# Performance work log

Measured on AMD Instinct MI355X. Metric: run time of the kernel, lower is better.

The kernel has to match this reference:

```python
import jax, jax.numpy as jnp
import numpy as np

B, N, K, E, H, V = 128, 256, 4, 300, 150, 32000  # batch, nodes/tree, max children, embed, hidden, vocab
DELTA = 1.0


def setup_inputs() -> dict:
    key = jax.random.key(0)
    ks = jax.random.split(key, 8)
    query = jax.random.randint(ks[0], (B, N), 0, V, dtype=jnp.int32)
    pos = jax.random.randint(ks[1], (B, N), 0, V, dtype=jnp.int32)
    neg = jax.random.randint(ks[2], (B, N), 0, V, dtype=jnp.int32)
    # Complete K-ary tree over N nodes: children of node t are {K*t+1, ..., K*t+K} < N; root = node 0.
    ch = np.full((N, K), -1, dtype=np.int32)
    for t in range(N):
        for j in range(K):
            c = K * t + 1 + j
            if c < N:
                ch[t, j] = c
    children = jnp.asarray(ch)
    emb = jax.random.normal(ks[3], (V, E), dtype=jnp.float32) * 0.02
    W_iou = jax.random.normal(ks[4], (E, 3 * H), dtype=jnp.float32) * 0.05
    U_iou = jax.random.normal(ks[5], (H, 3 * H), dtype=jnp.float32) * 0.05
    b_iou = jnp.zeros((3 * H,), jnp.float32)
    W_f = jax.random.normal(ks[6], (E, H), dtype=jnp.float32) * 0.05
    U_f = jax.random.normal(ks[7], (H, H), dtype=jnp.float32) * 0.05
    b_f = jnp.zeros((H,), jnp.float32)
    return {"query": query, "pos": pos, "neg": neg, "children": children,
            "emb": emb, "W_iou": W_iou, "U_iou": U_iou, "b_iou": b_iou,
            "W_f": W_f, "U_f": U_f, "b_f": b_f}


def _childsum_treelstm(x, children, W_iou, U_iou, b_iou, W_f, U_f, b_f):
    """x: [B, N, E] node embeddings. Returns root (c, h): each [B, H]."""
    Bn, Nn, _ = x.shape
    Hh = U_f.shape[0]
    h0 = jnp.zeros((Bn, Nn, Hh), x.dtype)
    c0 = jnp.zeros((Bn, Nn, Hh), x.dtype)

    def step(carry, t):
        h_all, c_all = carry
        ch = children[t]                        # [K] child indices, -1 = padding
        mask = (ch >= 0)
        idx = jnp.where(mask, ch, 0)
        m = mask.astype(x.dtype)[None, :, None]  # [1, K, 1]
        h_k = h_all[:, idx] * m                 # [B, K, H]
        c_k = c_all[:, idx] * m
        h_sum = h_k.sum(axis=1)                 # child-sum h_tilde [B, H]
        x_t = x[:, t]                           # [B, E]
        iou = x_t @ W_iou + h_sum @ U_iou + b_iou
        i, o, u = jnp.split(iou, 3, axis=-1)
        i = jax.nn.sigmoid(i)
        o = jax.nn.sigmoid(o)
        u = jnp.tanh(u)
        # per-child forget gates: f_jk = sigmoid(W_f x_j + U_f h_k + b_f)
        f = jax.nn.sigmoid((x_t @ W_f + b_f)[:, None, :] + h_k @ U_f)  # [B, K, H]
        c_t = i * u + (f * c_k).sum(axis=1)     # c_k already masked
        h_t = o * jnp.tanh(c_t)
        return (h_all.at[:, t].set(h_t), c_all.at[:, t].set(c_t)), None

    # children have larger indices than parents -> process N-1 .. 0 (root last)
    (h_all, c_all), _ = jax.lax.scan(step, (h0, c0), jnp.arange(Nn - 1, -1, -1))
    return c_all[:, 0], h_all[:, 0]


def _cosine(a, b):
    num = (a * b).sum(-1)
    den = jnp.sqrt((a * a).sum(-1) * (b * b).sum(-1)) + 1e-8
    return num / den


def reference(query, pos, neg, children, emb, W_iou, U_iou, b_iou, W_f, U_f, b_f):
    qc, _ = _childsum_treelstm(emb[query], children, W_iou, U_iou, b_iou, W_f, U_f, b_f)
    pc, _ = _childsum_treelstm(emb[pos], children, W_iou, U_iou, b_iou, W_f, U_f, b_f)
    nc, _ = _childsum_treelstm(emb[neg], children, W_iou, U_iou, b_iou, W_f, U_f, b_f)
    a = _cosine(qc, pc)  # [B]
    b = _cosine(qc, nc)  # [B]
    return jax.nn.relu(DELTA - a + b)
```

## Files before the change

kernel.cpp:

```cpp
#include <hip/hip_runtime.h>
#include <hip/hip_bf16.h>

typedef short short8 __attribute__((ext_vector_type(8)));
typedef float floatx4 __attribute__((ext_vector_type(4)));
typedef unsigned short ushort;

#define Bb 128
#define Nn 256
#define Hh 150
#define HK 160
#define Vv 32000
#define NROW 384
#define PROJC 600
#define NINT 64
#define ZROW (Vv + NROW * NINT)

#define WTN 640

__device__ __forceinline__ float sigf(float x) { return 1.0f / (1.0f + __expf(-x)); }
__device__ __forceinline__ float tanhf_(float x) { return 1.0f - 2.0f / (__expf(2.0f * x) + 1.0f); }
__device__ __forceinline__ float bf2f(ushort s) { union { float f; unsigned u; } v; v.u = ((unsigned)s) << 16; return v.f; }
__device__ __forceinline__ ushort f2bf(float f) { __hip_bfloat16 h = __float2bfloat16(f); return *(ushort*)&h; }

__global__ __launch_bounds__(256) void k_prep(
    const float* __restrict__ W_iou, const float* __restrict__ W_f,
    const float* __restrict__ U_iou, const float* __restrict__ U_f,
    const float* __restrict__ b_iou, const float* __restrict__ b_f,
    short* __restrict__ Wt, short* __restrict__ Uti, short* __restrict__ Utf,
    float* __restrict__ biasw, ushort* __restrict__ h_u, float* __restrict__ c_u)
{
    int idx = blockIdx.x * 256 + threadIdx.x;
    const int nWt = 320 * WTN, nUi = 160 * 464, nUf = 160 * 160;
    if (idx < nWt) {
        int k = idx / WTN, n = idx % WTN;
        float v = 0.f;
        if (k < 300) { if (n < 450) v = W_iou[k * 450 + n]; else if (n < 600) v = W_f[k * 150 + (n - 450)]; }
        Wt[n * 320 + k] = (short)f2bf(v);
    } else if (idx < nWt + nUi) {
        int i2 = idx - nWt; int k = i2 / 464, n = i2 % 464;
        float v = (k < 150 && n < 450) ? U_iou[k * 450 + n] : 0.f;
        Uti[n * 160 + k] = (short)f2bf(v);
    } else if (idx < nWt + nUi + nUf) {
        int i2 = idx - nWt - nUi; int k = i2 / 160, n = i2 % 160;
        float v = (k < 150 && n < 150) ? U_f[k * 150 + n] : 0.f;
        Utf[n * 160 + k] = (short)f2bf(v);
    } else if (idx < nWt + nUi + nUf + WTN) {
        int n = idx - nWt - nUi - nUf;
        biasw[n] = n < 450 ? b_iou[n] : (n < 600 ? b_f[n - 450] : 0.f);
    } else if (idx < nWt + nUi + nUf + WTN + HK) {
        int k = idx - (nWt + nUi + nUf + WTN);
        h_u[(long)ZROW * HK + k] = 0;
        c_u[(long)ZROW * HK + k] = 0.f;
    }
}

__global__ __launch_bounds__(256) void k_vproj(
    const float* __restrict__ emb, const short* __restrict__ Wt,
    const float* __restrict__ biasw, ushort* __restrict__ proj)
{
    __shared__ __align__(16) short As[2][32][328];
    const int tid = threadIdx.x;

    const int bid = blockIdx.x;
    const int xcd = bid & 7, li = bid >> 3;
    const int wgid = (xcd < 4 ? xcd * 63 : 252 + (xcd - 4) * 62) + li;

    const int cg = wgid % 5;
    const int rg = wgid / 5;
    const int rowbase = rg * 320;

    const int w = tid >> 6, lane = tid & 63;
    const int m = lane & 15, kq = (lane >> 4) * 8;
    const int t0 = cg * 8 + w * 2;
    const int col0 = t0 * 16 + m;
    const int col1 = col0 + 16;

    short8 bq0[10], bq1[10];
    #pragma unroll
    for (int ks = 0; ks < 10; ks++) {
        bq0[ks] = *(const short8*)(Wt + (long)col0 * 320 + kq + ks * 32);
        bq1[ks] = *(const short8*)(Wt + (long)col1 * 320 + kq + ks * 32);
    }
    const float bias0 = biasw[col0];
    const float bias1 = biasw[col1];

    for (int i = tid; i < 2 * 32 * 5; i += 256) {
        int bz = i / 160, r2 = (i % 160) / 5, kk = (i % 5) * 4;
        *(short4*)&As[bz][r2][300 + kk] = make_short4(0, 0, 0, 0);
    }

    {
        const float4* src = (const float4*)emb + (long)rowbase * 75;
        for (int i = tid; i < 2400; i += 256) {
            int r = i / 75, k0 = (i % 75) * 4;
            float4 x = src[i];
            short4 sv;
            sv.x = (short)f2bf(x.x); sv.y = (short)f2bf(x.y);
            sv.z = (short)f2bf(x.z); sv.w = (short)f2bf(x.w);
            *(short4*)&As[0][r][k0] = sv;
        }
    }
    __syncthreads();

    for (int c = 0; c < 10; c++) {
        const int buf = c & 1;

        float4 x[10];
        if (c < 9) {
            const float4* src = (const float4*)emb + (long)(rowbase + (c + 1) * 32) * 75;
            #pragma unroll
            for (int j = 0; j < 10; j++) {
                int i = tid + j * 256;
                if (i < 2400) x[j] = src[i];
            }
        }

        floatx4 a00 = {0.f,0.f,0.f,0.f}, a01 = a00, a10 = a00, a11 = a00;
        #pragma unroll
        for (int ks = 0; ks < 10; ks++) {
            short8 a0 = *(const short8*)&As[buf][m][kq + ks * 32];
            short8 a1 = *(const short8*)&As[buf][16 + m][kq + ks * 32];
            a00 = __builtin_amdgcn_mfma_f32_16x16x32_bf16(a0, bq0[ks], a00, 0, 0, 0);
            a01 = __builtin_amdgcn_mfma_f32_16x16x32_bf16(a0, bq1[ks], a01, 0, 0, 0);
            a10 = __builtin_amdgcn_mfma_f32_16x16x32_bf16(a1, bq0[ks], a10, 0, 0, 0);
            a11 = __builtin_amdgcn_mfma_f32_16x16x32_bf16(a1, bq1[ks], a11, 0, 0, 0);
        }

        {
            int v0 = rowbase + c * 32;
            int rb = (lane >> 4) * 4;
            if (col0 < PROJC) {
                #pragma unroll
                for (int reg = 0; reg < 4; reg++) {
                    proj[(long)(v0 + rb + reg) * PROJC + col0]      = f2bf(a00[reg] + bias0);
                    proj[(long)(v0 + 16 + rb + reg) * PROJC + col0] = f2bf(a10[reg] + bias0);
                }
            }
            if (col1 < PROJC) {
                #pragma unroll
                for (int reg = 0; reg < 4; reg++) {
                    proj[(long)(v0 + rb + reg) * PROJC + col1]      = f2bf(a01[reg] + bias1);
                    proj[(long)(v0 + 16 + rb + reg) * PROJC + col1] = f2bf(a11[reg] + bias1);
                }
            }
        }

        if (c < 9) {
            #pragma unroll
            for (int j = 0; j < 10; j++) {
                int i = tid + j * 256;
                if (i < 2400) {
                    int r = i / 75, k0 = (i % 75) * 4;
                    short4 sv;
                    sv.x = (short)f2bf(x[j].x); sv.y = (short)f2bf(x[j].y);
                    sv.z = (short)f2bf(x[j].z); sv.w = (short)f2bf(x[j].w);
                    *(short4*)&As[buf ^ 1][r][k0] = sv;
                }
            }
        }
        __syncthreads();
    }
}

__global__ __launch_bounds__(256) void k_vleaf(
    const ushort* __restrict__ proj, ushort* __restrict__ h_u, float* __restrict__ c_u)
{
    int idx = blockIdx.x * 256 + threadIdx.x;
    int v = idx / 20, k0 = (idx % 20) * 8;
    const ushort* pr = proj + (long)v * PROJC;
    ushort hv[8]; float cvv[8];
    #pragma unroll
    for (int e = 0; e < 8; e++) {
        int k = k0 + e;
        if (k < Hh) {
            float iv = sigf(bf2f(pr[k]));
            float ov = sigf(bf2f(pr[150 + k]));
            float uv = tanhf_(bf2f(pr[300 + k]));
            float cc = iv * uv;
            cvv[e] = cc;
            hv[e] = f2bf(ov * tanhf_(cc));
        } else { cvv[e] = 0.f; hv[e] = 0; }
    }
    *(int4*)(h_u + (long)v * HK + k0) = *(int4*)hv;
    *(float4*)(c_u + (long)v * HK + k0)     = make_float4(cvv[0], cvv[1], cvv[2], cvv[3]);
    *(float4*)(c_u + (long)v * HK + k0 + 4) = make_float4(cvv[4], cvv[5], cvv[6], cvv[7]);
}

template<int CB>
__device__ __forceinline__ void level_step(
    int tA, int nT, int r0, int cb,
    const int* __restrict__ tq, const int* __restrict__ tp, const int* __restrict__ tn,
    const int* __restrict__ children, const ushort* __restrict__ proj,
    const short* __restrict__ Uti, const short* __restrict__ Utf,
    ushort* __restrict__ h_u, float* __restrict__ c_u,
    short (*As)[16][168], ushort (*idx_s)[16][4], ushort (*tok_s)[16])
{
    const int tid = threadIdx.x;

    if (tid < 64 * nT) {
        int tt = tid >> 6, q = tid & 63;
        int r = q >> 2, j = q & 3;
        int t = tA + tt;
        int rg = r0 + r, g = rg >> 7, b = rg & 127;
        const int* tok = (g == 0) ? tq : (g == 1 ? tp : tn);
        int ch = children[t * 4 + j];
        int idx;
        if (ch < 0)        idx = ZROW;
        else if (ch >= 64) idx = tok[b * Nn + ch];
        else               idx = Vv + rg * NINT + ch;
        idx_s[tt][r][j] = (ushort)idx;
        if (j == 0) tok_s[tt][r] = (ushort)tok[b * Nn + t];
    }
    __syncthreads();

    for (int i = tid; i < 320 * nT; i += 256) {
        int tt = i / 320, i2 = i % 320;
        int r = i2 / 20, k0 = (i2 % 20) * 8;
        int4 v0 = *(const int4*)(h_u + (long)idx_s[tt][r][0] * HK + k0);
        int4 v1 = *(const int4*)(h_u + (long)idx_s[tt][r][1] * HK + k0);
        int4 v2 = *(const int4*)(h_u + (long)idx_s[tt][r][2] * HK + k0);
        int4 v3 = *(const int4*)(h_u + (long)idx_s[tt][r][3] * HK + k0);
        *(int4*)&As[tt * 5 + 1][r][k0] = v0;
        *(int4*)&As[tt * 5 + 2][r][k0] = v1;
        *(int4*)&As[tt * 5 + 3][r][k0] = v2;
        *(int4*)&As[tt * 5 + 4][r][k0] = v3;
        ushort s[8];
        const ushort* p0 = (const ushort*)&v0; const ushort* p1 = (const ushort*)&v1;
        const ushort* p2 = (const ushort*)&v2; const ushort* p3 = (const ushort*)&v3;
        #pragma unroll
        for (int e = 0; e < 8; e++)
            s[e] = f2bf(bf2f(p0[e]) + bf2f(p1[e]) + bf2f(p2[e]) + bf2f(p3[e]));
        *(int4*)&As[tt * 5 + 0][r][k0] = *(int4*)s;
    }
    __syncthreads();

    const int w = tid >> 6, lane = tid & 63;
    const int m = lane & 15, kq = (lane >> 4) * 8;
    const int rbase = (lane >> 4) * 4;

    for (int nt = w + 4 * cb; nt < 10; nt += 4 * CB) {
        int col = nt * 16 + m;

        short8 Bi[5], Bo[5], Bu[5], Bf[5];
        #pragma unroll
        for (int ks = 0; ks < 5; ks++) {
            Bi[ks] = *(const short8*)(Uti + (long)(col)       * HK + kq + ks * 32);
            Bo[ks] = *(const short8*)(Uti + (long)(150 + col) * HK + kq + ks * 32);
            Bu[ks] = *(const short8*)(Uti + (long)(300 + col) * HK + kq + ks * 32);
            Bf[ks] = *(const short8*)(Utf + (long)(col)       * HK + kq + ks * 32);
        }

        for (int tt = 0; tt < nT; ++tt) {
            int t = tA + tt;

            float pv0[4], pv1[4], pv2[4], pv3[4];
            float cu0[4], cu1[4], cu2[4], cu3[4];
            if (col < Hh) {
                #pragma unroll
                for (int reg = 0; reg < 4; reg++) {
                    const ushort* pr = proj + (long)tok_s[tt][rbase + reg] * PROJC;
                    pv0[reg] = bf2f(pr[col]);
                    pv1[reg] = bf2f(pr[150 + col]);
                    pv2[reg] = bf2f(pr[300 + col]);
                    pv3[reg] = bf2f(pr[450 + col]);
                    cu0[reg] = c_u[(long)idx_s[tt][rbase + reg][0] * HK + col];
                    cu1[reg] = c_u[(long)idx_s[tt][rbase + reg][1] * HK + col];
                    cu2[reg] = c_u[(long)idx_s[tt][rbase + reg][2] * HK + col];
                    cu3[reg] = c_u[(long)idx_s[tt][rbase + reg][3] * HK + col];
                }
            }

            floatx4 ai = {0.f,0.f,0.f,0.f}, ao = ai, au = ai;
            floatx4 af0 = ai, af1 = ai, af2 = ai, af3 = ai;
            #pragma unroll
            for (int ks = 0; ks < 5; ks++) {
                short8 asum = *(const short8*)&As[tt * 5 + 0][m][kq + ks * 32];
                short8 ac0  = *(const short8*)&As[tt * 5 + 1][m][kq + ks * 32];
                short8 ac1  = *(const short8*)&As[tt * 5 + 2][m][kq + ks * 32];
                short8 ac2  = *(const short8*)&As[tt * 5 + 3][m][kq + ks * 32];
                short8 ac3  = *(const short8*)&As[tt * 5 + 4][m][kq + ks * 32];
                ai  = __builtin_amdgcn_mfma_f32_16x16x32_bf16(asum, Bi[ks], ai, 0, 0, 0);
                ao  = __builtin_amdgcn_mfma_f32_16x16x32_bf16(asum, Bo[ks], ao, 0, 0, 0);
                au  = __builtin_amdgcn_mfma_f32_16x16x32_bf16(asum, Bu[ks], au, 0, 0, 0);
                af0 = __builtin_amdgcn_mfma_f32_16x16x32_bf16(ac0,  Bf[ks], af0, 0, 0, 0);
                af1 = __builtin_amdgcn_mfma_f32_16x16x32_bf16(ac1,  Bf[ks], af1, 0, 0, 0);
                af2 = __builtin_amdgcn_mfma_f32_16x16x32_bf16(ac2,  Bf[ks], af2, 0, 0, 0);
                af3 = __builtin_amdgcn_mfma_f32_16x16x32_bf16(ac3,  Bf[ks], af3, 0, 0, 0);
            }

            if (col < Hh) {
                #pragma unroll
                for (int reg = 0; reg < 4; reg++) {
                    int rg = r0 + rbase + reg;
                    float iv = sigf(pv0[reg] + ai[reg]);
                    float ov = sigf(pv1[reg] + ao[reg]);
                    float uv = tanhf_(pv2[reg] + au[reg]);
                    float fpre = pv3[reg];
                    float cv = iv * uv;
                    cv = fmaf(sigf(fpre + af0[reg]), cu0[reg], cv);
                    cv = fmaf(sigf(fpre + af1[reg]), cu1[reg], cv);
                    cv = fmaf(sigf(fpre + af2[reg]), cu2[reg], cv);
                    cv = fmaf(sigf(fpre + af3[reg]), cu3[reg], cv);
                    long o = (long)(Vv + rg * NINT + t) * HK + col;
                    c_u[o] = cv;
                    h_u[o] = f2bf(ov * tanhf_(cv));
                }
            } else {
                #pragma unroll
                for (int reg = 0; reg < 4; reg++) {
                    long o = (long)(Vv + (r0 + rbase + reg) * NINT + t) * HK + col;
                    c_u[o] = 0.f; h_u[o] = 0;
                }
            }
        }
    }
}

template<int CB>
__global__ __launch_bounds__(256) void k_level(
    int t_base, int t_cnt,
    const int* __restrict__ tq, const int* __restrict__ tp, const int* __restrict__ tn,
    const int* __restrict__ children, const ushort* __restrict__ proj,
    const short* __restrict__ Uti, const short* __restrict__ Utf,
    ushort* __restrict__ h_u, float* __restrict__ c_u)
{
    __shared__ __align__(16) short As[10][16][168];
    __shared__ ushort idx_s[2][16][4];
    __shared__ ushort tok_s[2][16];

    const int chunk = blockIdx.x / (24 * CB);
    const int rem   = blockIdx.x % (24 * CB);
    const int r0 = (rem / CB) * 16;
    const int cb = rem % CB;
    const int tA = t_base + chunk * 2;
    const int nT = min(2, t_base + t_cnt - tA);

    level_step<CB>(tA, nT, r0, cb, tq, tp, tn, children, proj, Uti, Utf,
                   h_u, c_u, As, idx_s, tok_s);
}

__global__ __launch_bounds__(64) void k_cos(const float* __restrict__ c_u, float* __restrict__ out)
{
    int b = blockIdx.x, tid = threadIdx.x;
    const float* qc = c_u + (long)(Vv + (0 * Bb + b) * NINT) * HK;
    const float* pc = c_u + (long)(Vv + (1 * Bb + b) * NINT) * HK;
    const float* nc = c_u + (long)(Vv + (2 * Bb + b) * NINT) * HK;
    float qp = 0, qn = 0, qq = 0, pp = 0, nn2 = 0;
    for (int k = tid; k < Hh; k += 64) {
        float qv = qc[k], pv = pc[k], nv = nc[k];
        qp += qv * pv; qn += qv * nv; qq += qv * qv; pp += pv * pv; nn2 += nv * nv;
    }
    #pragma unroll
    for (int off = 32; off > 0; off >>= 1) {
        qp += __shfl_down(qp, off, 64);
        qn += __shfl_down(qn, off, 64);
        qq += __shfl_down(qq, off, 64);
        pp += __shfl_down(pp, off, 64);
        nn2 += __shfl_down(nn2, off, 64);
    }
    if (tid == 0) {
        float a = qp / (sqrtf(qq * pp) + 1e-8f);
        float d = qn / (sqrtf(qq * nn2) + 1e-8f);
        out[b] = fmaxf(0.0f, 1.0f - a + d);
    }
}

extern "C" void kernel_launch(void* const* d_in, const int* in_sizes, int n_in,
                              void* d_out, int out_size, void* d_ws, size_t ws_size,
                              hipStream_t stream)
{
    const int*   tq       = (const int*)d_in[0];
    const int*   tp       = (const int*)d_in[1];
    const int*   tn       = (const int*)d_in[2];
    const int*   children = (const int*)d_in[3];
    const float* emb      = (const float*)d_in[4];
    const float* W_iou    = (const float*)d_in[5];
    const float* U_iou    = (const float*)d_in[6];
    const float* b_iou    = (const float*)d_in[7];
    const float* W_f      = (const float*)d_in[8];
    const float* U_f      = (const float*)d_in[9];
    const float* b_f      = (const float*)d_in[10];
    float* out = (float*)d_out;

    char* ws = (char*)d_ws;
    ushort* proj  = (ushort*)ws;
    ushort* h_u   = (ushort*)(ws + 38400000);
    float*  c_u   = (float*)(ws + 56504640);
    short*  Wt    = (short*)(ws + 92713920);
    short*  Uti   = (short*)(ws + 93123520);
    short*  Utf   = (short*)(ws + 93272000);
    float*  biasw = (float*)(ws + 93323200);

    k_prep<<<1194, 256, 0, stream>>>(W_iou, W_f, U_iou, U_f, b_iou, b_f,
                                     Wt, Uti, Utf, biasw, h_u, c_u);
    k_vproj<<<500, 256, 0, stream>>>(emb, Wt, biasw, proj);
    k_vleaf<<<2500, 256, 0, stream>>>(proj, h_u, c_u);
    k_level<1><<<22 * 24, 256, 0, stream>>>(21, 43, tq, tp, tn, children, proj, Uti, Utf, h_u, c_u);
    k_level<1><<<8 * 24, 256, 0, stream>>>(5, 16, tq, tp, tn, children, proj, Uti, Utf, h_u, c_u);
    k_level<2><<<2 * 24 * 2, 256, 0, stream>>>(1, 4, tq, tp, tn, children, proj, Uti, Utf, h_u, c_u);
    k_level<2><<<1 * 24 * 2, 256, 0, stream>>>(0, 1, tq, tp, tn, children, proj, Uti, Utf, h_u, c_u);
    k_cos<<<Bb, 64, 0, stream>>>(c_u, out);
}
```

Before: 240.8 us.

## Interleave projection gate columns and fuse leaf LSTM cell into vocab projection GEMM

Reorders the projected weight columns so the i/o/u/f gates of each hidden unit sit next to each other. The vocab-projection kernel can then compute leaf cell and hidden states in its epilogue using lane shuffles, and the separate leaf kernel and its re-read of the projection table are removed. The level kernel now reads all four gate values for a node with one short4 load instead of four scattered loads. The cost is extra transcendental work and scattered 4-byte stores in the GEMM epilogue, which could lengthen that kernel.

```diff
diff --git a/kernel.cpp b/kernel.cpp
--- a/kernel.cpp
+++ b/kernel.cpp
@@ -17,6 +17,7 @@
 
 #define WTN 640
 
+
 __device__ __forceinline__ float sigf(float x) { return 1.0f / (1.0f + __expf(-x)); }
 __device__ __forceinline__ float tanhf_(float x) { return 1.0f - 2.0f / (__expf(2.0f * x) + 1.0f); }
 __device__ __forceinline__ float bf2f(ushort s) { union { float f; unsigned u; } v; v.u = ((unsigned)s) << 16; return v.f; }
@@ -32,10 +33,12 @@
     int idx = blockIdx.x * 256 + threadIdx.x;
     const int nWt = 320 * WTN, nUi = 160 * 464, nUf = 160 * 160;
     if (idx < nWt) {
-        int k = idx / WTN, n = idx % WTN;
+        int kk = idx / WTN, c = idx % WTN;
+        int k = c >> 2, g = c & 3;
         float v = 0.f;
-        if (k < 300) { if (n < 450) v = W_iou[k * 450 + n]; else if (n < 600) v = W_f[k * 150 + (n - 450)]; }
-        Wt[n * 320 + k] = (short)f2bf(v);
+        if (kk < 300 && k < 150)
+            v = (g < 3) ? W_iou[kk * 450 + g * 150 + k] : W_f[kk * 150 + k];
+        Wt[c * 320 + kk] = (short)f2bf(v);
     } else if (idx < nWt + nUi) {
         int i2 = idx - nWt; int k = i2 / 464, n = i2 % 464;
         float v = (k < 150 && n < 450) ? U_iou[k * 450 + n] : 0.f;
@@ -45,8 +48,9 @@
         float v = (k < 150 && n < 150) ? U_f[k * 150 + n] : 0.f;
         Utf[n * 160 + k] = (short)f2bf(v);
     } else if (idx < nWt + nUi + nUf + WTN) {
-        int n = idx - nWt - nUi - nUf;
-        biasw[n] = n < 450 ? b_iou[n] : (n < 600 ? b_f[n - 450] : 0.f);
+        int c = idx - nWt - nUi - nUf;
+        int k = c >> 2, g = c & 3;
+        biasw[c] = (k < 150) ? (g < 3 ? b_iou[g * 150 + k] : b_f[k]) : 0.f;
     } else if (idx < nWt + nUi + nUf + WTN + HK) {
         int k = idx - (nWt + nUi + nUf + WTN);
         h_u[(long)ZROW * HK + k] = 0;
@@ -56,7 +60,8 @@
 
 __global__ __launch_bounds__(256) void k_vproj(
     const float* __restrict__ emb, const short* __restrict__ Wt,
-    const float* __restrict__ biasw, ushort* __restrict__ proj)
+    const float* __restrict__ biasw, ushort* __restrict__ proj,
+    ushort* __restrict__ h_u, float* __restrict__ c_u)
 {
     __shared__ __align__(16) short As[2][32][328];
     const int tid = threadIdx.x;
@@ -74,6 +79,9 @@
     const int t0 = cg * 8 + w * 2;
     const int col0 = t0 * 16 + m;
     const int col1 = col0 + 16;
+    const int g = m & 3;
+    const int k0 = t0 * 4 + (m >> 2);
+    const int rb = (lane >> 4) * 4;
 
     short8 bq0[10], bq1[10];
     #pragma unroll
@@ -92,12 +100,12 @@
     {
         const float4* src = (const float4*)emb + (long)rowbase * 75;
         for (int i = tid; i < 2400; i += 256) {
-            int r = i / 75, k0 = (i % 75) * 4;
+            int r = i / 75, kk0 = (i % 75) * 4;
             float4 x = src[i];
             short4 sv;
             sv.x = (short)f2bf(x.x); sv.y = (short)f2bf(x.y);
             sv.z = (short)f2bf(x.z); sv.w = (short)f2bf(x.w);
-            *(short4*)&As[0][r][k0] = sv;
+            *(short4*)&As[0][r][kk0] = sv;
         }
     }
     __syncthreads();
@@ -126,9 +134,9 @@
             a11 = __builtin_amdgcn_mfma_f32_16x16x32_bf16(a1, bq1[ks], a11, 0, 0, 0);
         }
 
+        const int v0 = rowbase + c * 32;
+
         {
-            int v0 = rowbase + c * 32;
-            int rb = (lane >> 4) * 4;
             if (col0 < PROJC) {
                 #pragma unroll
                 for (int reg = 0; reg < 4; reg++) {
@@ -145,45 +153,60 @@
             }
         }
 
+        #pragma unroll
+        for (int reg = 0; reg < 4; reg++) {
+            float vA = a00[reg] + bias0;
+            float vB = a10[reg] + bias0;
+            float vC = a01[reg] + bias1;
+            float vD = a11[reg] + bias1;
+            float A1 = __shfl_xor(vA, 1), A2 = __shfl_xor(vA, 2), A3 = __shfl_xor(vA, 3);
+            float B1 = __shfl_xor(vB, 1), B2 = __shfl_xor(vB, 2), B3 = __shfl_xor(vB, 3);
+            float C1 = __shfl_xor(vC, 1), C2 = __shfl_xor(vC, 2), C3 = __shfl_xor(vC, 3);
+            float D1 = __shfl_xor(vD, 1), D2 = __shfl_xor(vD, 2), D3 = __shfl_xor(vD, 3);
+            if (g < 2) {
+                int r0w = v0 + rb + reg, r1w = v0 + 16 + rb + reg;
+                {
+                    float iv = g ? A1 : vA, ov = g ? vA : A1, uv = g ? A3 : A2;
+                    float cc = sigf(iv) * tanhf_(uv);
+                    if (g == 0) c_u[(long)r0w * HK + k0] = cc;
+                    else        h_u[(long)r0w * HK + k0] = f2bf(sigf(ov) * tanhf_(cc));
+                }
+                {
+                    float iv = g ? B1 : vB, ov = g ? vB : B1, uv = g ? B3 : B2;
+                    float cc = sigf(iv) * tanhf_(uv);
+                    if (g == 0) c_u[(long)r1w * HK + k0] = cc;
+                    else        h_u[(long)r1w * HK + k0] = f2bf(sigf(ov) * tanhf_(cc));
+                }
+                {
+                    float iv = g ? C1 : vC, ov = g ? vC : C1, uv = g ? C3 : C2;
+                    float cc = sigf(iv) * tanhf_(uv);
+                    if (g == 0) c_u[(long)r0w * HK + k0 + 4] = cc;
+                    else        h_u[(long)r0w * HK + k0 + 4] = f2bf(sigf(ov) * tanhf_(cc));
+                }
+                {
+                    float iv = g ? D1 : vD, ov = g ? vD : D1, uv = g ? D3 : D2;
+                    float cc = sigf(iv) * tanhf_(uv);
+                    if (g == 0) c_u[(long)r1w * HK + k0 + 4] = cc;
+                    else        h_u[(long)r1w * HK + k0 + 4] = f2bf(sigf(ov) * tanhf_(cc));
+                }
+            }
+        }
+
         if (c < 9) {
             #pragma unroll
             for (int j = 0; j < 10; j++) {
                 int i = tid + j * 256;
                 if (i < 2400) {
-                    int r = i / 75, k0 = (i % 75) * 4;
+                    int r = i / 75, kk0 = (i % 75) * 4;
                     short4 sv;
                     sv.x = (short)f2bf(x[j].x); sv.y = (short)f2bf(x[j].y);
                     sv.z = (short)f2bf(x[j].z); sv.w = (short)f2bf(x[j].w);
-                    *(short4*)&As[buf ^ 1][r][k0] = sv;
+                    *(short4*)&As[buf ^ 1][r][kk0] = sv;
                 }
             }
         }
         __syncthreads();
     }
-}
-
-__global__ __launch_bounds__(256) void k_vleaf(
-    const ushort* __restrict__ proj, ushort* __restrict__ h_u, float* __restrict__ c_u)
-{
-    int idx = blockIdx.x * 256 + threadIdx.x;
-    int v = idx / 20, k0 = (idx % 20) * 8;
-    const ushort* pr = proj + (long)v * PROJC;
-    ushort hv[8]; float cvv[8];
-    #pragma unroll
-    for (int e = 0; e < 8; e++) {
-        int k = k0 + e;
-        if (k < Hh) {
-            float iv = sigf(bf2f(pr[k]));
-            float ov = sigf(bf2f(pr[150 + k]));
-            float uv = tanhf_(bf2f(pr[300 + k]));
-            float cc = iv * uv;
-            cvv[e] = cc;
-            hv[e] = f2bf(ov * tanhf_(cc));
-        } else { cvv[e] = 0.f; hv[e] = 0; }
-    }
-    *(int4*)(h_u + (long)v * HK + k0) = *(int4*)hv;
-    *(float4*)(c_u + (long)v * HK + k0)     = make_float4(cvv[0], cvv[1], cvv[2], cvv[3]);
-    *(float4*)(c_u + (long)v * HK + k0 + 4) = make_float4(cvv[4], cvv[5], cvv[6], cvv[7]);
 }
 
 template<int CB>
@@ -259,10 +282,11 @@
                 #pragma unroll
                 for (int reg = 0; reg < 4; reg++) {
                     const ushort* pr = proj + (long)tok_s[tt][rbase + reg] * PROJC;
-                    pv0[reg] = bf2f(pr[col]);
-                    pv1[reg] = bf2f(pr[150 + col]);
-                    pv2[reg] = bf2f(pr[300 + col]);
-                    pv3[reg] = bf2f(pr[450 + col]);
+                    short4 q4 = *(const short4*)(pr + 4 * col);
+                    pv0[reg] = bf2f((ushort)q4.x);
+                    pv1[reg] = bf2f((ushort)q4.y);
+                    pv2[reg] = bf2f((ushort)q4.z);
+                    pv3[reg] = bf2f((ushort)q4.w);
                     cu0[reg] = c_u[(long)idx_s[tt][rbase + reg][0] * HK + col];
                     cu1[reg] = c_u[(long)idx_s[tt][rbase + reg][1] * HK + col];
                     cu2[reg] = c_u[(long)idx_s[tt][rbase + reg][2] * HK + col];
@@ -393,8 +417,7 @@
 
     k_prep<<<1194, 256, 0, stream>>>(W_iou, W_f, U_iou, U_f, b_iou, b_f,
                                      Wt, Uti, Utf, biasw, h_u, c_u);
-    k_vproj<<<500, 256, 0, stream>>>(emb, Wt, biasw, proj);
-    k_vleaf<<<2500, 256, 0, stream>>>(proj, h_u, c_u);
+    k_vproj<<<500, 256, 0, stream>>>(emb, Wt, biasw, proj, h_u, c_u);
     k_level<1><<<22 * 24, 256, 0, stream>>>(21, 43, tq, tp, tn, children, proj, Uti, Utf, h_u, c_u);
     k_level<1><<<8 * 24, 256, 0, stream>>>(5, 16, tq, tp, tn, children, proj, Uti, Utf, h_u, c_u);
     k_level<2><<<2 * 24 * 2, 256, 0, stream>>>(1, 4, tq, tp, tn, children, proj, Uti, Utf, h_u, c_u);
```

New measurement: 257.4 us. +6.9%, slower.
